# Kernel tuning notes

Measured on AMD Instinct MI355X. Metric: run time of the kernel, lower is better.

The kernel has to match this reference:

```python
import jax, jax.numpy as jnp
import numpy as np

HIDDEN = 2048
N_HEADS = 16
Q_DIM = N_HEADS * 128  # 2048
INTER = 10944
EPS = 1e-6
B, S = 2, 2048


def rms_norm(x, w, eps):
    var = jnp.mean(jnp.square(x), axis=-1, keepdims=True)
    return x * jax.lax.rsqrt(var + eps) * w


def setup_inputs() -> dict:
    key = jax.random.key(0)
    ks = jax.random.split(key, 8)
    x = jax.random.normal(ks[0], (B, S, HIDDEN), dtype=jnp.float32)
    positions = jnp.broadcast_to(jnp.arange(S, dtype=jnp.int32), (B, S))
    sc = 0.02
    return {
        "x": x,
        "positions": positions,
        "in_w": jnp.ones((HIDDEN,), dtype=jnp.float32),
        "post_w": jnp.ones((HIDDEN,), dtype=jnp.float32),
        "Wq": jax.random.normal(ks[1], (Q_DIM, HIDDEN), dtype=jnp.float32) * sc,
        "Wo": jax.random.normal(ks[2], (HIDDEN, Q_DIM), dtype=jnp.float32) * sc,
        "Wg": jax.random.normal(ks[3], (INTER, HIDDEN), dtype=jnp.float32) * sc,
        "Wu": jax.random.normal(ks[4], (INTER, HIDDEN), dtype=jnp.float32) * sc,
        "Wd": jax.random.normal(ks[5], (HIDDEN, INTER), dtype=jnp.float32) * sc,
    }


def reference(x, positions, in_w, post_w, Wq, Wo, Wg, Wu, Wd):
    b, s, h = x.shape
    xf = x.reshape(-1, h)                       # [T, H]
    h_norm = rms_norm(xf, in_w, EPS)            # RMSNorm (input_layernorm)
    q = jnp.einsum('th,qh->tq', h_norm, Wq)     # q_proj
    hidden = xf + jnp.einsum('tq,hq->th', q, Wo)  # o_proj + residual
    h_post = rms_norm(hidden, post_w, EPS)      # post_attention_layernorm
    gate = jax.nn.silu(jnp.einsum('th,ih->ti', h_post, Wg))
    up = jnp.einsum('th,ih->ti', h_post, Wu)
    mlp = jnp.einsum('ti,hi->th', gate * up, Wd)  # down_proj
    return (hidden + mlp).reshape(b, s, h)
```

## Files before the change

kernel.cpp:

```cpp
#include <hip/hip_runtime.h>
#include <hip/hip_bf16.h>
#include <stdint.h>


typedef __bf16 bf16;
typedef bf16 bf16x8 __attribute__((ext_vector_type(8)));
typedef bf16 bf16x4 __attribute__((ext_vector_type(4)));
typedef float f32x4 __attribute__((ext_vector_type(4)));

#define HID     2048
#define TOK     4096
#define INTER   10944
#define INTER_P 11008
#define BK      32

__device__ __forceinline__ void gload_lds16(const bf16* g, bf16* l) {
    __builtin_amdgcn_global_load_lds(
        (const __attribute__((address_space(1))) void*)g,
        (__attribute__((address_space(3))) void*)l, 16, 0, 0);
}

__global__ __launch_bounds__(256) void conv_pad(const float* __restrict__ src,
                                                bf16* __restrict__ dst,
                                                int n_src, int n_dst) {
    int i = (blockIdx.x * 256 + threadIdx.x) * 4;
    if (i >= n_dst) return;
    float4 v = make_float4(0.f, 0.f, 0.f, 0.f);
    if (i < n_src) v = *(const float4*)(src + i);
    bf16x4 o;
    o[0] = (bf16)v.x; o[1] = (bf16)v.y; o[2] = (bf16)v.z; o[3] = (bf16)v.w;
    *(bf16x4*)(dst + i) = o;
}

__global__ __launch_bounds__(256) void conv_wd(const float* __restrict__ src,
                                               bf16* __restrict__ dst) {
    int i = (blockIdx.x * 256 + threadIdx.x) * 4;
    if (i >= HID * INTER_P) return;
    int row = i / INTER_P;
    int col = i - row * INTER_P;
    float4 v = make_float4(0.f, 0.f, 0.f, 0.f);
    if (col < INTER)
        v = *(const float4*)(src + (size_t)row * INTER + col);
    bf16x4 o;
    o[0] = (bf16)v.x; o[1] = (bf16)v.y; o[2] = (bf16)v.z; o[3] = (bf16)v.w;
    *(bf16x4*)(dst + i) = o;
}

__global__ __launch_bounds__(256) void rmsnorm_k(const float* __restrict__ x,
                                                 const float* __restrict__ w,
                                                 bf16* __restrict__ out) {
    const int row = blockIdx.x;
    const int tid = threadIdx.x;
    const float* xr = x + (size_t)row * HID + tid * 8;
    float4 v0 = *(const float4*)(xr);
    float4 v1 = *(const float4*)(xr + 4);
    float s = v0.x * v0.x + v0.y * v0.y + v0.z * v0.z + v0.w * v0.w +
              v1.x * v1.x + v1.y * v1.y + v1.z * v1.z + v1.w * v1.w;
    #pragma unroll
    for (int o = 32; o > 0; o >>= 1) s += __shfl_down(s, o);
    __shared__ float red[4];
    if ((tid & 63) == 0) red[tid >> 6] = s;
    __syncthreads();
    float tot = red[0] + red[1] + red[2] + red[3];
    float scale = rsqrtf(tot * (1.0f / (float)HID) + 1e-6f);
    float4 w0 = *(const float4*)(w + tid * 8);
    float4 w1 = *(const float4*)(w + tid * 8 + 4);
    bf16x8 o8;
    o8[0] = (bf16)(v0.x * scale * w0.x);
    o8[1] = (bf16)(v0.y * scale * w0.y);
    o8[2] = (bf16)(v0.z * scale * w0.z);
    o8[3] = (bf16)(v0.w * scale * w0.w);
    o8[4] = (bf16)(v1.x * scale * w1.x);
    o8[5] = (bf16)(v1.y * scale * w1.y);
    o8[6] = (bf16)(v1.z * scale * w1.z);
    o8[7] = (bf16)(v1.w * scale * w1.w);
    *(bf16x8*)(out + (size_t)row * HID + tid * 8) = o8;
}

template <int EPI>
__global__ __launch_bounds__(512, 4) void gemm_bt5(const bf16* __restrict__ A,
                                                   const bf16* __restrict__ W,
                                                   const float* __restrict__ res,
                                                   void* __restrict__ out,
                                                   int N, int K) {
    __shared__ bf16 lA[128 * BK];
    __shared__ bf16 lW[128 * BK];
    const int tid = threadIdx.x;
    const int rowBase = blockIdx.x * 128;
    const int colBase = blockIdx.y * 128;
    const int wave = tid >> 6, lane = tid & 63;
    const int wm = (wave >> 2) * 64, wn = (wave & 3) * 32;
    const int lr = lane & 15, kq = lane >> 4;

    f32x4 acc[4][2] = {};
    const bf16* Ab = A + (size_t)rowBase * K;
    const bf16* Wb = W + (size_t)colBase * K;

    const int sr = tid >> 2;
    const int ss = (tid & 3) ^ ((sr >> 1) & 3);
    const size_t goff = (size_t)sr * K + ss * 8;

    int aoff[4], woff[2];
    #pragma unroll
    for (int i = 0; i < 4; ++i) {
        int r = wm + i * 16 + lr;
        aoff[i] = r * BK + (kq ^ ((r >> 1) & 3)) * 8;
    }
    #pragma unroll
    for (int i = 0; i < 2; ++i) {
        int r = wn + i * 16 + lr;
        woff[i] = r * BK + (kq ^ ((r >> 1) & 3)) * 8;
    }

    for (int k0 = 0; k0 < K; k0 += BK) {
        gload_lds16(Ab + goff + k0, &lA[tid * 8]);
        gload_lds16(Wb + goff + k0, &lW[tid * 8]);
        __syncthreads();
        bf16x8 af[4], wf[2];
        #pragma unroll
        for (int i = 0; i < 4; ++i) af[i] = *(const bf16x8*)&lA[aoff[i]];
        #pragma unroll
        for (int i = 0; i < 2; ++i) wf[i] = *(const bf16x8*)&lW[woff[i]];
        #pragma unroll
        for (int mi = 0; mi < 4; ++mi)
            #pragma unroll
            for (int ni = 0; ni < 2; ++ni)
                acc[mi][ni] = __builtin_amdgcn_mfma_f32_16x16x32_bf16(
                    af[mi], wf[ni], acc[mi][ni], 0, 0, 0);
        __syncthreads();
    }
    const int rq = lane >> 4, cn = lane & 15;
    #pragma unroll
    for (int mi = 0; mi < 4; ++mi) {
        #pragma unroll
        for (int ni = 0; ni < 2; ++ni) {
            int col = colBase + wn + ni * 16 + cn;
            #pragma unroll
            for (int r = 0; r < 4; ++r) {
                int row = rowBase + wm + mi * 16 + rq * 4 + r;
                size_t idx = (size_t)row * N + col;
                float v = acc[mi][ni][r];
                if (EPI == 0) ((bf16*)out)[idx] = (bf16)v;
                else          ((float*)out)[idx] = res[idx] + v;
            }
        }
    }
}

__global__ __launch_bounds__(512, 4) void gemm_gu5(const bf16* __restrict__ A,
                                                   const bf16* __restrict__ Wg,
                                                   const bf16* __restrict__ Wu,
                                                   bf16* __restrict__ out,
                                                   int N, int K) {
    __shared__ bf16 lA[128 * BK];
    __shared__ bf16 lG[128 * BK];
    __shared__ bf16 lU[128 * BK];
    const int tid = threadIdx.x;
    const int rowBase = blockIdx.x * 128;
    const int colBase = blockIdx.y * 128;
    const int wave = tid >> 6, lane = tid & 63;
    const int wm = (wave >> 2) * 64, wn = (wave & 3) * 32;
    const int lr = lane & 15, kq = lane >> 4;

    f32x4 ag[4][2] = {};
    f32x4 au[4][2] = {};
    const bf16* Ab = A + (size_t)rowBase * K;
    const bf16* Gb = Wg + (size_t)colBase * K;
    const bf16* Ub = Wu + (size_t)colBase * K;

    const int sr = tid >> 2;
    const int ss = (tid & 3) ^ ((sr >> 1) & 3);
    const size_t goff = (size_t)sr * K + ss * 8;

    int aoff[4], boff[2];
    #pragma unroll
    for (int i = 0; i < 4; ++i) {
        int r = wm + i * 16 + lr;
        aoff[i] = r * BK + (kq ^ ((r >> 1) & 3)) * 8;
    }
    #pragma unroll
    for (int i = 0; i < 2; ++i) {
        int r = wn + i * 16 + lr;
        boff[i] = r * BK + (kq ^ ((r >> 1) & 3)) * 8;
    }

    for (int k0 = 0; k0 < K; k0 += BK) {
        gload_lds16(Ab + goff + k0, &lA[tid * 8]);
        gload_lds16(Gb + goff + k0, &lG[tid * 8]);
        gload_lds16(Ub + goff + k0, &lU[tid * 8]);
        __syncthreads();
        bf16x8 af[4], gf[2], uf[2];
        #pragma unroll
        for (int i = 0; i < 4; ++i) af[i] = *(const bf16x8*)&lA[aoff[i]];
        #pragma unroll
        for (int i = 0; i < 2; ++i) {
            gf[i] = *(const bf16x8*)&lG[boff[i]];
            uf[i] = *(const bf16x8*)&lU[boff[i]];
        }
        #pragma unroll
        for (int mi = 0; mi < 4; ++mi)
            #pragma unroll
            for (int ni = 0; ni < 2; ++ni) {
                ag[mi][ni] = __builtin_amdgcn_mfma_f32_16x16x32_bf16(
                    af[mi], gf[ni], ag[mi][ni], 0, 0, 0);
                au[mi][ni] = __builtin_amdgcn_mfma_f32_16x16x32_bf16(
                    af[mi], uf[ni], au[mi][ni], 0, 0, 0);
            }
        __syncthreads();
    }
    const int rq = lane >> 4, cn = lane & 15;
    #pragma unroll
    for (int mi = 0; mi < 4; ++mi) {
        #pragma unroll
        for (int ni = 0; ni < 2; ++ni) {
            int col = colBase + wn + ni * 16 + cn;
            #pragma unroll
            for (int r = 0; r < 4; ++r) {
                int row = rowBase + wm + mi * 16 + rq * 4 + r;
                float g = ag[mi][ni][r];
                float u = au[mi][ni][r];
                float sg = g / (1.0f + __expf(-g));
                out[(size_t)row * N + col] = (bf16)(sg * u);
            }
        }
    }
}

extern "C" void kernel_launch(void* const* d_in, const int* in_sizes, int n_in,
                              void* d_out, int out_size, void* d_ws, size_t ws_size,
                              hipStream_t stream) {
    const float* x      = (const float*)d_in[0];
    const float* in_w   = (const float*)d_in[2];
    const float* post_w = (const float*)d_in[3];
    const float* Wq     = (const float*)d_in[4];
    const float* Wo     = (const float*)d_in[5];
    const float* Wg     = (const float*)d_in[6];
    const float* Wu     = (const float*)d_in[7];
    const float* Wd     = (const float*)d_in[8];

    char* ws = (char*)d_ws;
    bf16*  X    = (bf16*)(ws + 0);
    bf16*  Yq   = (bf16*)(ws + 16777216);
    float* hid  = (float*)(ws + 33554432);
    bf16*  gu   = (bf16*)(ws + 67108864);
    bf16*  w0   = (bf16*)(ws + 157286400);
    bf16*  w1   = (bf16*)(ws + 202375168);
    bf16*  wsm  = (bf16*)(ws + 247463936);

    const int nGU  = INTER_P * HID;
    const int nGUs = INTER * HID;
    const int nSq  = HID * HID;

    conv_pad<<<nGU / 4 / 256, 256, 0, stream>>>(Wg, w0, nGUs, nGU);
    conv_pad<<<nGU / 4 / 256, 256, 0, stream>>>(Wu, w1, nGUs, nGU);
    conv_pad<<<nSq / 4 / 256, 256, 0, stream>>>(Wq, wsm, nSq, nSq);

    rmsnorm_k<<<TOK, 256, 0, stream>>>(x, in_w, X);
    gemm_bt5<0><<<dim3(TOK / 128, HID / 128), 512, 0, stream>>>(
        X, wsm, nullptr, Yq, HID, HID);
    conv_pad<<<nSq / 4 / 256, 256, 0, stream>>>(Wo, wsm, nSq, nSq);
    gemm_bt5<1><<<dim3(TOK / 128, HID / 128), 512, 0, stream>>>(
        Yq, wsm, x, hid, HID, HID);
    rmsnorm_k<<<TOK, 256, 0, stream>>>(hid, post_w, X);
    gemm_gu5<<<dim3(TOK / 128, INTER_P / 128), 512, 0, stream>>>(
        X, w0, w1, gu, INTER_P, HID);
    conv_wd<<<nGU / 4 / 256, 256, 0, stream>>>(Wd, w0);
    gemm_bt5<1><<<dim3(TOK / 128, HID / 128), 512, 0, stream>>>(
        gu, w0, hid, (float*)d_out, HID, INTER_P);
}
```

Baseline: 1.094 ms.

## Double-buffer GEMM LDS tiles with register-staged prefetch two steps ahead

Replaces direct global-to-LDS loads with global loads into registers issued two K-steps ahead, written into a double-buffered LDS tile after the MFMAs. Each K-step now needs one barrier instead of two. The aim is to hide global memory latency behind compute. In exchange it doubles LDS use, adds register pressure, and lowers the gate/up kernel's occupancy hint from 4 to 3.

```diff
diff --git a/kernel.cpp b/kernel.cpp
--- a/kernel.cpp
+++ b/kernel.cpp
@@ -14,10 +14,9 @@
 #define INTER_P 11008
 #define BK      32
 
-__device__ __forceinline__ void gload_lds16(const bf16* g, bf16* l) {
-    __builtin_amdgcn_global_load_lds(
-        (const __attribute__((address_space(1))) void*)g,
-        (__attribute__((address_space(3))) void*)l, 16, 0, 0);
+__device__ __forceinline__ void barrier_lgkm() {
+    __asm__ volatile("s_waitcnt lgkmcnt(0)" ::: "memory");
+    __builtin_amdgcn_s_barrier();
 }
 
 __global__ __launch_bounds__(256) void conv_pad(const float* __restrict__ src,
@@ -83,8 +82,8 @@
                                                    const float* __restrict__ res,
                                                    void* __restrict__ out,
                                                    int N, int K) {
-    __shared__ bf16 lA[128 * BK];
-    __shared__ bf16 lW[128 * BK];
+    __shared__ bf16 lA[2][128 * BK];
+    __shared__ bf16 lW[2][128 * BK];
     const int tid = threadIdx.x;
     const int rowBase = blockIdx.x * 128;
     const int colBase = blockIdx.y * 128;
@@ -93,12 +92,13 @@
     const int lr = lane & 15, kq = lane >> 4;
 
     f32x4 acc[4][2] = {};
-    const bf16* Ab = A + (size_t)rowBase * K;
-    const bf16* Wb = W + (size_t)colBase * K;
 
     const int sr = tid >> 2;
     const int ss = (tid & 3) ^ ((sr >> 1) & 3);
-    const size_t goff = (size_t)sr * K + ss * 8;
+    const bf16* Ag = A + (size_t)rowBase * K + (size_t)sr * K + ss * 8;
+    const bf16* Wg = W + (size_t)colBase * K + (size_t)sr * K + ss * 8;
+    bf16* ldA = &lA[0][0] + tid * 8;
+    bf16* ldW = &lW[0][0] + tid * 8;
 
     int aoff[4], woff[2];
     #pragma unroll
@@ -112,22 +112,42 @@
         woff[i] = r * BK + (kq ^ ((r >> 1) & 3)) * 8;
     }
 
-    for (int k0 = 0; k0 < K; k0 += BK) {
-        gload_lds16(Ab + goff + k0, &lA[tid * 8]);
-        gload_lds16(Wb + goff + k0, &lW[tid * 8]);
-        __syncthreads();
-        bf16x8 af[4], wf[2];
+    const int nk = K / BK;
+    uint4 sA[2], sW[2];
+    sA[0] = *(const uint4*)(Ag);
+    sW[0] = *(const uint4*)(Wg);
+    sA[1] = *(const uint4*)(Ag + BK);
+    sW[1] = *(const uint4*)(Wg + BK);
+    *(uint4*)ldA = sA[0];
+    *(uint4*)ldW = sW[0];
+    barrier_lgkm();
+
+    for (int j0 = 0; j0 < nk; j0 += 2) {
         #pragma unroll
-        for (int i = 0; i < 4; ++i) af[i] = *(const bf16x8*)&lA[aoff[i]];
-        #pragma unroll
-        for (int i = 0; i < 2; ++i) wf[i] = *(const bf16x8*)&lW[woff[i]];
-        #pragma unroll
-        for (int mi = 0; mi < 4; ++mi)
-            #pragma unroll
-            for (int ni = 0; ni < 2; ++ni)
-                acc[mi][ni] = __builtin_amdgcn_mfma_f32_16x16x32_bf16(
-                    af[mi], wf[ni], acc[mi][ni], 0, 0, 0);
-        __syncthreads();
+        for (int h = 0; h < 2; ++h) {
+            const int j = j0 + h;
+            const int k2 = (j + 2 < nk) ? (j + 2) * BK : 0;
+            sA[h] = *(const uint4*)(Ag + k2);
+            sW[h] = *(const uint4*)(Wg + k2);
+            const int cb = h * 128 * BK;
+            bf16x8 af[4], wf[2];
+            #pragma unroll
+            for (int i = 0; i < 4; ++i)
+                af[i] = *(const bf16x8*)&lA[0][cb + aoff[i]];
+            #pragma unroll
+            for (int i = 0; i < 2; ++i)
+                wf[i] = *(const bf16x8*)&lW[0][cb + woff[i]];
+            #pragma unroll
+            for (int mi = 0; mi < 4; ++mi)
+                #pragma unroll
+                for (int ni = 0; ni < 2; ++ni)
+                    acc[mi][ni] = __builtin_amdgcn_mfma_f32_16x16x32_bf16(
+                        af[mi], wf[ni], acc[mi][ni], 0, 0, 0);
+            const int nb = (h ^ 1) * 128 * BK * (int)sizeof(bf16);
+            *(uint4*)((char*)ldA + nb) = sA[h ^ 1];
+            *(uint4*)((char*)ldW + nb) = sW[h ^ 1];
+            barrier_lgkm();
+        }
     }
     const int rq = lane >> 4, cn = lane & 15;
     #pragma unroll
@@ -147,14 +167,14 @@
     }
 }
 
-__global__ __launch_bounds__(512, 4) void gemm_gu5(const bf16* __restrict__ A,
-                                                   const bf16* __restrict__ Wg,
-                                                   const bf16* __restrict__ Wu,
+__global__ __launch_bounds__(512, 3) void gemm_gu5(const bf16* __restrict__ A,
+                                                   const bf16* __restrict__ Wgp,
+                                                   const bf16* __restrict__ Wup,
                                                    bf16* __restrict__ out,
                                                    int N, int K) {
-    __shared__ bf16 lA[128 * BK];
-    __shared__ bf16 lG[128 * BK];
-    __shared__ bf16 lU[128 * BK];
+    __shared__ bf16 lA[2][128 * BK];
+    __shared__ bf16 lG[2][128 * BK];
+    __shared__ bf16 lU[2][128 * BK];
     const int tid = threadIdx.x;
     const int rowBase = blockIdx.x * 128;
     const int colBase = blockIdx.y * 128;
@@ -164,13 +184,15 @@
 
     f32x4 ag[4][2] = {};
     f32x4 au[4][2] = {};
-    const bf16* Ab = A + (size_t)rowBase * K;
-    const bf16* Gb = Wg + (size_t)colBase * K;
-    const bf16* Ub = Wu + (size_t)colBase * K;
 
     const int sr = tid >> 2;
     const int ss = (tid & 3) ^ ((sr >> 1) & 3);
-    const size_t goff = (size_t)sr * K + ss * 8;
+    const bf16* Ag = A   + (size_t)rowBase * K + (size_t)sr * K + ss * 8;
+    const bf16* Gg = Wgp + (size_t)colBase * K + (size_t)sr * K + ss * 8;
+    const bf16* Ug = Wup + (size_t)colBase * K + (size_t)sr * K + ss * 8;
+    bf16* ldA = &lA[0][0] + tid * 8;
+    bf16* ldG = &lG[0][0] + tid * 8;
+    bf16* ldU = &lU[0][0] + tid * 8;
 
     int aoff[4], boff[2];
     #pragma unroll
@@ -184,29 +206,52 @@
         boff[i] = r * BK + (kq ^ ((r >> 1) & 3)) * 8;
     }
 
-    for (int k0 = 0; k0 < K; k0 += BK) {
-        gload_lds16(Ab + goff + k0, &lA[tid * 8]);
-        gload_lds16(Gb + goff + k0, &lG[tid * 8]);
-        gload_lds16(Ub + goff + k0, &lU[tid * 8]);
-        __syncthreads();
-        bf16x8 af[4], gf[2], uf[2];
+    const int nk = K / BK;
+    uint4 sA[2], sG[2], sU[2];
+    sA[0] = *(const uint4*)(Ag);
+    sG[0] = *(const uint4*)(Gg);
+    sU[0] = *(const uint4*)(Ug);
+    sA[1] = *(const uint4*)(Ag + BK);
+    sG[1] = *(const uint4*)(Gg + BK);
+    sU[1] = *(const uint4*)(Ug + BK);
+    *(uint4*)ldA = sA[0];
+    *(uint4*)ldG = sG[0];
+    *(uint4*)ldU = sU[0];
+    barrier_lgkm();
+
+    for (int j0 = 0; j0 < nk; j0 += 2) {
         #pragma unroll
-        for (int i = 0; i < 4; ++i) af[i] = *(const bf16x8*)&lA[aoff[i]];
-        #pragma unroll
-        for (int i = 0; i < 2; ++i) {
-            gf[i] = *(const bf16x8*)&lG[boff[i]];
-            uf[i] = *(const bf16x8*)&lU[boff[i]];
+        for (int h = 0; h < 2; ++h) {
+            const int j = j0 + h;
+            const int k2 = (j + 2 < nk) ? (j + 2) * BK : 0;
+            sA[h] = *(const uint4*)(Ag + k2);
+            sG[h] = *(const uint4*)(Gg + k2);
+            sU[h] = *(const uint4*)(Ug + k2);
+            const int cb = h * 128 * BK;
+            bf16x8 af[4], gf[2], uf[2];
+            #pragma unroll
+            for (int i = 0; i < 4; ++i)
+                af[i] = *(const bf16x8*)&lA[0][cb + aoff[i]];
+            #pragma unroll
+            for (int i = 0; i < 2; ++i) {
+                gf[i] = *(const bf16x8*)&lG[0][cb + boff[i]];
+                uf[i] = *(const bf16x8*)&lU[0][cb + boff[i]];
+            }
+            #pragma unroll
+            for (int mi = 0; mi < 4; ++mi)
+                #pragma unroll
+                for (int ni = 0; ni < 2; ++ni) {
+                    ag[mi][ni] = __builtin_amdgcn_mfma_f32_16x16x32_bf16(
+                        af[mi], gf[ni], ag[mi][ni], 0, 0, 0);
+                    au[mi][ni] = __builtin_amdgcn_mfma_f32_16x16x32_bf16(
+                        af[mi], uf[ni], au[mi][ni], 0, 0, 0);
+                }
+            const int nb = (h ^ 1) * 128 * BK * (int)sizeof(bf16);
+            *(uint4*)((char*)ldA + nb) = sA[h ^ 1];
+            *(uint4*)((char*)ldG + nb) = sG[h ^ 1];
+            *(uint4*)((char*)ldU + nb) = sU[h ^ 1];
+            barrier_lgkm();
         }
-        #pragma unroll
-        for (int mi = 0; mi < 4; ++mi)
-            #pragma unroll
-            for (int ni = 0; ni < 2; ++ni) {
-                ag[mi][ni] = __builtin_amdgcn_mfma_f32_16x16x32_bf16(
-                    af[mi], gf[ni], ag[mi][ni], 0, 0, 0);
-                au[mi][ni] = __builtin_amdgcn_mfma_f32_16x16x32_bf16(
-                    af[mi], uf[ni], au[mi][ni], 0, 0, 0);
-            }
-        __syncthreads();
     }
     const int rq = lane >> 4, cn = lane & 15;
     #pragma unroll
```

Result: slower. 1.948 ms (+78.1%).
